# Optimization experiments

Measured on AMD Instinct MI355X. Metric: run time of the kernel, lower is better.

Reference implementation:

```python
import jax, jax.numpy as jnp
import numpy as np

H = 4096      # hidden_size
NH = 32       # num query heads
NKV = 2       # multi_query_group_num (kv heads)
HD = 128      # head_dim
ROT = 64      # rotary_dim = head_dim // 2
B, S = 2, 2048
QKV = (NH + 2 * NKV) * HD  # 4608
BASE = 10000.0


def apply_rope(x, pos):
    """GPT-J style (non-neox, interleaved) rope on first ROT dims of head_dim.
    x: [B,S,n,HD], pos: [B,S] int."""
    half = ROT // 2  # 32 frequency pairs
    inv_freq = 1.0 / (BASE ** (jnp.arange(0, ROT, 2, dtype=jnp.float32) / ROT))  # [half]
    freqs = pos.astype(jnp.float32)[..., None] * inv_freq        # [B,S,half]
    cos = jnp.cos(freqs)[:, :, None, :]                          # [B,S,1,half]
    sin = jnp.sin(freqs)[:, :, None, :]
    xr, xp = x[..., :ROT], x[..., ROT:]
    x1 = xr[..., 0::2]   # [B,S,n,half]
    x2 = xr[..., 1::2]
    o1 = x1 * cos - x2 * sin
    o2 = x2 * cos + x1 * sin
    rot = jnp.stack([o1, o2], axis=-1).reshape(x.shape[:-1] + (ROT,))
    return jnp.concatenate([rot, xp], axis=-1)


def setup_inputs() -> dict:
    key = jax.random.key(0)
    k1, k2, k3, k4 = jax.random.split(key, 4)
    hidden_states = jax.random.normal(k1, (B, S, H), dtype=jnp.float32)
    position_ids = jnp.broadcast_to(jnp.arange(S, dtype=jnp.int64), (B, S))
    Wqkv = jax.random.normal(k2, (H, QKV), dtype=jnp.float32) * 0.02
    bqkv = jax.random.normal(k3, (QKV,), dtype=jnp.float32) * 0.02
    Wo = jax.random.normal(k4, (NH * HD, H), dtype=jnp.float32) * 0.02
    return {"hidden_states": hidden_states, "position_ids": position_ids,
            "Wqkv": Wqkv, "bqkv": bqkv, "Wo": Wo}


def reference(hidden_states, position_ids, Wqkv, bqkv, Wo):
    qkv = hidden_states @ Wqkv + bqkv                      # [B,S,QKV]
    q = qkv[..., : NH * HD].reshape(B, S, NH, HD)
    k = qkv[..., NH * HD : (NH + NKV) * HD].reshape(B, S, NKV, HD)
    v = qkv[..., (NH + NKV) * HD :].reshape(B, S, NKV, HD)

    q = apply_rope(q, position_ids)
    k = apply_rope(k, position_ids)

    # GQA: expand kv heads to match query heads
    rep = NH // NKV
    k = jnp.repeat(k, rep, axis=2)   # [B,S,NH,HD]
    v = jnp.repeat(v, rep, axis=2)

    scale = HD ** -0.5
    scores = jnp.einsum("bqhd,bkhd->bhqk", q, k) * scale   # [B,NH,S,S]
    causal = jnp.tril(jnp.ones((S, S), dtype=bool))
    scores = jnp.where(causal, scores, jnp.finfo(scores.dtype).min)
    probs = jax.nn.softmax(scores, axis=-1)
    ctx = jnp.einsum("bhqk,bkhd->bqhd", probs, v).reshape(B, S, NH * HD)
    return ctx @ Wo                                        # [B,S,H]
```

## Files before the change

### kernel.cpp

```cpp
#include <hip/hip_runtime.h>
#include <stdint.h>

#define B_    2
#define S_    2048
#define H_    4096
#define NH_   32
#define NKV_  2
#define HD_   128
#define ROT_  64
#define QKVD  4608
#define MROWS 4096

typedef __attribute__((ext_vector_type(8))) __bf16 bf16x8;
typedef __attribute__((ext_vector_type(4))) float f32x4;

__device__ __forceinline__ unsigned short f2bf(float f) {
    union { float f; unsigned u; } c; c.f = f;
    unsigned u = c.u;
    u += 0x7fffu + ((u >> 16) & 1u);
    return (unsigned short)(u >> 16);
}

__device__ __forceinline__ void gload_lds16(const void* g, void* l) {
    __builtin_amdgcn_global_load_lds(
        (__attribute__((address_space(1))) void*)g,
        (__attribute__((address_space(3))) void*)l, 16, 0, 0);
}

__global__ __launch_bounds__(256) void convert_bf16(const float* __restrict__ src,
                                                    unsigned short* __restrict__ dst,
                                                    int n4) {
    int i = blockIdx.x * 256 + threadIdx.x;
    if (i < n4) {
        f32x4 v = ((const f32x4*)src)[i];
        ushort4 o;
        o.x = f2bf(v[0]); o.y = f2bf(v[1]); o.z = f2bf(v[2]); o.w = f2bf(v[3]);
        ((ushort4*)dst)[i] = o;
    }
}

__global__ __launch_bounds__(256) void transpose_bf16(const float* __restrict__ src,
                                                      unsigned short* __restrict__ dst,
                                                      int K, int N) {
    __shared__ float tile[32][33];
    int n0 = blockIdx.x * 32, k0 = blockIdx.y * 32;
    int tx = threadIdx.x & 31, ty = threadIdx.x >> 5;
#pragma unroll
    for (int i = 0; i < 4; i++)
        tile[ty + i * 8][tx] = src[(size_t)(k0 + ty + i * 8) * N + n0 + tx];
    __syncthreads();
#pragma unroll
    for (int i = 0; i < 4; i++)
        dst[(size_t)(n0 + ty + i * 8) * K + k0 + tx] = f2bf(tile[tx][ty + i * 8]);
}

template <int HAS_BIAS>
__global__ __launch_bounds__(256) void gemm_bt(const unsigned short* __restrict__ A,
                                               const unsigned short* __restrict__ BT,
                                               const float* __restrict__ bias,
                                               float* __restrict__ C,
                                               int M, int N, int K) {
    __shared__ __align__(16) unsigned short As[128 * 32];
    __shared__ __align__(16) unsigned short Bs[128 * 32];
    int tid = threadIdx.x;
    int lane = tid & 63, wave = tid >> 6;
    int quad = lane >> 4, lrow = lane & 15;
    int m0 = blockIdx.y * 128, n0 = blockIdx.x * 128;
    int wm = (wave >> 1) * 64, wn = (wave & 1) * 64;

    f32x4 acc[4][4];
#pragma unroll
    for (int mt = 0; mt < 4; mt++)
#pragma unroll
        for (int nt = 0; nt < 4; nt++) acc[mt][nt] = (f32x4){0.f, 0.f, 0.f, 0.f};

    int li0 = tid, li1 = 256 + tid;
    const unsigned short* ga0 = A + (size_t)(m0 + (li0 >> 2)) * K + (li0 & 3) * 8;
    const unsigned short* ga1 = A + (size_t)(m0 + (li1 >> 2)) * K + (li1 & 3) * 8;
    const unsigned short* gb0 = BT + (size_t)(n0 + (li0 >> 2)) * K + (li0 & 3) * 8;
    const unsigned short* gb1 = BT + (size_t)(n0 + (li1 >> 2)) * K + (li1 & 3) * 8;
    unsigned short* la0 = &As[(li0 & ~63) * 8];
    unsigned short* la1 = &As[(li1 & ~63) * 8];
    unsigned short* lb0 = &Bs[(li0 & ~63) * 8];
    unsigned short* lb1 = &Bs[(li1 & ~63) * 8];

    for (int k0 = 0; k0 < K; k0 += 32) {
        gload_lds16(ga0 + k0, la0);
        gload_lds16(ga1 + k0, la1);
        gload_lds16(gb0 + k0, lb0);
        gload_lds16(gb1 + k0, lb1);
        __syncthreads();
        bf16x8 af[4], bfr[4];
#pragma unroll
        for (int mt = 0; mt < 4; mt++)
            af[mt] = *(const bf16x8*)&As[(wm + mt * 16 + lrow) * 32 + quad * 8];
#pragma unroll
        for (int nt = 0; nt < 4; nt++)
            bfr[nt] = *(const bf16x8*)&Bs[(wn + nt * 16 + lrow) * 32 + quad * 8];
#pragma unroll
        for (int mt = 0; mt < 4; mt++)
#pragma unroll
            for (int nt = 0; nt < 4; nt++)
                acc[mt][nt] = __builtin_amdgcn_mfma_f32_16x16x32_bf16(af[mt], bfr[nt],
                                                                      acc[mt][nt], 0, 0, 0);
        __syncthreads();
    }
#pragma unroll
    for (int mt = 0; mt < 4; mt++) {
        int gm = m0 + wm + mt * 16 + quad * 4;
#pragma unroll
        for (int nt = 0; nt < 4; nt++) {
            int gn = n0 + wn + nt * 16 + lrow;
            float bv = HAS_BIAS ? bias[gn] : 0.f;
#pragma unroll
            for (int r = 0; r < 4; r++)
                C[(size_t)(gm + r) * N + gn] = acc[mt][nt][r] + bv;
        }
    }
}

__global__ __launch_bounds__(256) void gemm_qkv(const unsigned short* __restrict__ A,
                                                const unsigned short* __restrict__ BT,
                                                const float* __restrict__ bias,
                                                unsigned short* __restrict__ Qb,
                                                unsigned short* __restrict__ Kb,
                                                unsigned short* __restrict__ Vb) {
    const int K = H_;
    __shared__ __align__(16) unsigned short As[128 * 32];
    __shared__ __align__(16) unsigned short Bs[128 * 32];
    int tid = threadIdx.x;
    int lane = tid & 63, wave = tid >> 6;
    int quad = lane >> 4, lrow = lane & 15;
    int m0 = blockIdx.y * 128, n0 = blockIdx.x * 128;
    int head = blockIdx.x;
    int wm = (wave >> 1) * 64, wn = (wave & 1) * 64;

    f32x4 acc[4][4];
#pragma unroll
    for (int mt = 0; mt < 4; mt++)
#pragma unroll
        for (int nt = 0; nt < 4; nt++) acc[mt][nt] = (f32x4){0.f, 0.f, 0.f, 0.f};

    int li0 = tid, li1 = 256 + tid;
    const unsigned short* ga0 = A + (size_t)(m0 + (li0 >> 2)) * K + (li0 & 3) * 8;
    const unsigned short* ga1 = A + (size_t)(m0 + (li1 >> 2)) * K + (li1 & 3) * 8;
    const unsigned short* gb0 = BT + (size_t)(n0 + (li0 >> 2)) * K + (li0 & 3) * 8;
    const unsigned short* gb1 = BT + (size_t)(n0 + (li1 >> 2)) * K + (li1 & 3) * 8;
    unsigned short* la0 = &As[(li0 & ~63) * 8];
    unsigned short* la1 = &As[(li1 & ~63) * 8];
    unsigned short* lb0 = &Bs[(li0 & ~63) * 8];
    unsigned short* lb1 = &Bs[(li1 & ~63) * 8];

    for (int k0 = 0; k0 < K; k0 += 32) {
        gload_lds16(ga0 + k0, la0);
        gload_lds16(ga1 + k0, la1);
        gload_lds16(gb0 + k0, lb0);
        gload_lds16(gb1 + k0, lb1);
        __syncthreads();
        bf16x8 af[4], bfr[4];
#pragma unroll
        for (int mt = 0; mt < 4; mt++)
            af[mt] = *(const bf16x8*)&As[(wm + mt * 16 + lrow) * 32 + quad * 8];
#pragma unroll
        for (int nt = 0; nt < 4; nt++)
            bfr[nt] = *(const bf16x8*)&Bs[(wn + nt * 16 + lrow) * 32 + quad * 8];
#pragma unroll
        for (int mt = 0; mt < 4; mt++)
#pragma unroll
            for (int nt = 0; nt < 4; nt++)
                acc[mt][nt] = __builtin_amdgcn_mfma_f32_16x16x32_bf16(af[mt], bfr[nt],
                                                                      acc[mt][nt], 0, 0, 0);
        __syncthreads();
    }

    const float QSCALE = 0.08838834764831843f * 1.4426950408889634f;
#pragma unroll
    for (int mt = 0; mt < 4; mt++) {
        int gm = m0 + wm + mt * 16 + quad * 4;
        int bb = gm >> 11;
        int srow = gm & (S_ - 1);
#pragma unroll
        for (int nt = 0; nt < 4; nt++) {
            int dcol = wn + nt * 16 + lrow;
            float bv = bias[n0 + dcol];
            float vals[4];
#pragma unroll
            for (int r = 0; r < 4; r++) vals[r] = acc[mt][nt][r] + bv;
            if (head < 34 && dcol < ROT_) {
                int p = dcol >> 1;
                float inv = exp2f(-(float)p * 0.41524101186092035f);
                int odd = dcol & 1;
#pragma unroll
                for (int r = 0; r < 4; r++) {
                    float partner = __shfl_xor(vals[r], 1);
                    float sn, cs;
                    __sincosf((float)(srow + r) * inv, &sn, &cs);
                    vals[r] = odd ? (vals[r] * cs + partner * sn)
                                  : (vals[r] * cs - partner * sn);
                }
            }
            if (head < 32) {
                unsigned short* dst =
                    Qb + ((size_t)(bb * NH_ + head) * S_ + srow) * HD_ + dcol;
#pragma unroll
                for (int r = 0; r < 4; r++) dst[r * HD_] = f2bf(vals[r] * QSCALE);
            } else if (head < 34) {
                size_t base = ((size_t)(bb * NKV_ + head - 32) * S_ + srow) * HD_;
#pragma unroll
                for (int r = 0; r < 4; r++)
                    Kb[base + r * HD_ + (((dcol >> 3) ^ ((srow + r) & 7)) << 3) +
                       (dcol & 7)] = f2bf(vals[r]);
            } else {
                size_t base = ((size_t)(bb * NKV_ + head - 34) * HD_ + dcol) * S_;
#pragma unroll
                for (int r = 0; r < 4; r++) {
                    int s = srow + r;
                    Vb[base + ((s >> 6) << 6) + ((((s >> 3) & 7) ^ (dcol & 7)) << 3) +
                       (s & 7)] = f2bf(vals[r]);
                }
            }
        }
    }
}

__global__ __launch_bounds__(256, 4) void flash4(const unsigned short* __restrict__ Qb,
                                                 const unsigned short* __restrict__ Kb,
                                                 const unsigned short* __restrict__ Vb,
                                                 unsigned short* __restrict__ ctxb) {
    int pair = blockIdx.x;
    int h = blockIdx.y, b = blockIdx.z;
    int tid = threadIdx.x, lane = tid & 63, wave = tid >> 6;
    int quad = lane >> 4, lrow = lane & 15;
    int bkvh = b * NKV_ + (h >> 4);
    int lw3 = lrow & 7;

    __shared__ __align__(16) unsigned short Ks[64 * 128];
    __shared__ __align__(16) unsigned short Vt[128 * 64];
    __shared__ __align__(16) unsigned short Ps[4][16 * 64];

    const unsigned short* Kg = Kb + (size_t)bkvh * S_ * HD_;
    const unsigned short* Vg = Vb + (size_t)bkvh * HD_ * S_;

#pragma unroll 1
    for (int u = 0; u < 2; u++) {
        int qblk = u ? ((int)(S_ / 64) - 1 - pair) : pair;
        int q0 = qblk * 64 + wave * 16;

        bf16x8 qf[4];
        {
            const unsigned short* qr =
                Qb + ((size_t)(b * NH_ + h) * S_ + q0 + lrow) * HD_ + quad * 8;
#pragma unroll
            for (int c = 0; c < 4; c++) qf[c] = *(const bf16x8*)(qr + c * 32);
        }

        float m_i[4], l_i[4];
        f32x4 oacc[8];
#pragma unroll
        for (int r = 0; r < 4; r++) { m_i[r] = -1e30f; l_i[r] = 0.f; }
#pragma unroll
        for (int t = 0; t < 8; t++) oacc[t] = (f32x4){0.f, 0.f, 0.f, 0.f};

        int nkt = qblk + 1;
#pragma unroll 1
        for (int kt = 0; kt < nkt; kt++) {
            int ks0 = kt * 64;
            {
                const unsigned short* g =
                    Kg + (size_t)(ks0 + wave * 16 + (lane >> 4)) * HD_ + (lane & 15) * 8;
                unsigned short* l = &Ks[wave * 16 * 128];
#pragma unroll
                for (int i = 0; i < 4; i++)
                    gload_lds16(g + i * 4 * 128, l + i * 4 * 128);
            }
            {
                const unsigned short* g =
                    Vg + (size_t)(wave * 32 + (lane >> 3)) * S_ + ks0 + (lane & 7) * 8;
                unsigned short* l = &Vt[wave * 32 * 64];
#pragma unroll
                for (int i = 0; i < 4; i++)
                    gload_lds16(g + (size_t)i * 8 * S_, l + i * 8 * 64);
            }
            __syncthreads();

            if (ks0 <= q0 + 15) {
                f32x4 s[4];
#pragma unroll
                for (int n = 0; n < 4; n++) s[n] = (f32x4){0.f, 0.f, 0.f, 0.f};
#pragma unroll
                for (int kc = 0; kc < 4; kc++)
#pragma unroll
                    for (int n = 0; n < 4; n++) {
                        bf16x8 kf = *(const bf16x8*)
                            &Ks[(n * 16 + lrow) * 128 + (((kc * 4 + quad) ^ lw3) << 3)];
                        s[n] = __builtin_amdgcn_mfma_f32_16x16x32_bf16(qf[kc], kf, s[n],
                                                                       0, 0, 0);
                    }
                if (kt == nkt - 1) {
#pragma unroll
                    for (int n = 0; n < 4; n++)
#pragma unroll
                        for (int r = 0; r < 4; r++)
                            if (ks0 + n * 16 + lrow > q0 + quad * 4 + r)
                                s[n][r] = -1e30f;
                }
                float alpha[4];
#pragma unroll
                for (int r = 0; r < 4; r++) {
                    float mx = fmaxf(fmaxf(s[0][r], s[1][r]), fmaxf(s[2][r], s[3][r]));
                    mx = fmaxf(mx, __shfl_xor(mx, 1));
                    mx = fmaxf(mx, __shfl_xor(mx, 2));
                    mx = fmaxf(mx, __shfl_xor(mx, 4));
                    mx = fmaxf(mx, __shfl_xor(mx, 8));
                    float mn = fmaxf(m_i[r], mx);
                    alpha[r] = exp2f(m_i[r] - mn);
                    m_i[r] = mn;
                    float rs = 0.f;
#pragma unroll
                    for (int n = 0; n < 4; n++) {
                        s[n][r] = exp2f(s[n][r] - mn);
                        rs += s[n][r];
                    }
                    rs += __shfl_xor(rs, 1);
                    rs += __shfl_xor(rs, 2);
                    rs += __shfl_xor(rs, 4);
                    rs += __shfl_xor(rs, 8);
                    l_i[r] = l_i[r] * alpha[r] + rs;
                }
#pragma unroll
                for (int n = 0; n < 4; n++)
#pragma unroll
                    for (int r = 0; r < 4; r++) {
                        int rw = quad * 4 + r, col = n * 16 + lrow;
                        Ps[wave][rw * 64 + (((col >> 3) ^ (rw & 7)) << 3) + (col & 7)] =
                            f2bf(s[n][r]);
                    }
#pragma unroll
                for (int t = 0; t < 8; t++)
#pragma unroll
                    for (int r = 0; r < 4; r++) oacc[t][r] *= alpha[r];
                bf16x8 pf0 = *(const bf16x8*)&Ps[wave][lrow * 64 + ((quad ^ lw3) << 3)];
                bf16x8 pf1 = *(const bf16x8*)&Ps[wave][lrow * 64 + (((4 + quad) ^ lw3) << 3)];
#pragma unroll
                for (int t = 0; t < 8; t++) {
                    int dim = t * 16 + lrow;
                    bf16x8 v0 = *(const bf16x8*)&Vt[dim * 64 + ((quad ^ lw3) << 3)];
                    bf16x8 v1 = *(const bf16x8*)&Vt[dim * 64 + (((4 + quad) ^ lw3) << 3)];
                    oacc[t] = __builtin_amdgcn_mfma_f32_16x16x32_bf16(pf0, v0, oacc[t], 0, 0, 0);
                    oacc[t] = __builtin_amdgcn_mfma_f32_16x16x32_bf16(pf1, v1, oacc[t], 0, 0, 0);
                }
            }
            __syncthreads();
        }
        float inv[4];
#pragma unroll
        for (int r = 0; r < 4; r++) inv[r] = 1.f / l_i[r];
#pragma unroll
        for (int t = 0; t < 8; t++)
#pragma unroll
            for (int r = 0; r < 4; r++) {
                int q = q0 + quad * 4 + r;
                ctxb[(size_t)(b * S_ + q) * (NH_ * HD_) + h * HD_ + t * 16 + lrow] =
                    f2bf(oacc[t][r] * inv[r]);
            }
    }
}

extern "C" void kernel_launch(void* const* d_in, const int* in_sizes, int n_in,
                              void* d_out, int out_size, void* d_ws, size_t ws_size,
                              hipStream_t stream) {
    const float* hidden = (const float*)d_in[0];
    const float* Wqkv = (const float*)d_in[2];
    const float* bqkv = (const float*)d_in[3];
    const float* Wo   = (const float*)d_in[4];
    float* out = (float*)d_out;

    char* ws = (char*)d_ws;
    unsigned short* Xb    = (unsigned short*)ws;
    unsigned short* WqkvT = (unsigned short*)(ws + 33554432);
    unsigned short* Qb    = (unsigned short*)(ws + 71303168);
    unsigned short* Kb    = (unsigned short*)(ws + 104857600);
    unsigned short* Vb    = (unsigned short*)(ws + 106954752);
    unsigned short* ctxb  = (unsigned short*)(ws + 109051904);
    unsigned short* WoT   = Xb;

    convert_bf16<<<16384, 256, 0, stream>>>(hidden, Xb, (MROWS * H_) / 4);
    transpose_bf16<<<dim3(QKVD / 32, H_ / 32), 256, 0, stream>>>(Wqkv, WqkvT, H_, QKVD);
    gemm_qkv<<<dim3(QKVD / 128, MROWS / 128), 256, 0, stream>>>(Xb, WqkvT, bqkv,
                                                                Qb, Kb, Vb);
    transpose_bf16<<<dim3(H_ / 32, H_ / 32), 256, 0, stream>>>(Wo, WoT, NH_ * HD_, H_);
    flash4<<<dim3(S_ / 128, NH_, B_), 256, 0, stream>>>(Qb, Kb, Vb, ctxb);
    gemm_bt<0><<<dim3(H_ / 128, MROWS / 128), 256, 0, stream>>>(ctxb, WoT, nullptr, out,
                                                                MROWS, H_, NH_ * HD_);
}
```

Measured before the change: 837.7 us.

## Replace both GEMMs with 256x256 tiled, multi-buffered pipelined MFMA kernel

Both projection GEMMs are replaced by one templated kernel that uses 256x256 block tiles, 512 threads and 128KB of dynamic LDS. The K tile grows to 64 with an XOR-swizzled layout to avoid bank conflicts. Global-to-LDS loads for later K steps are issued while MFMAs run on the current buffers, with explicit vmcnt waits, barriers and setprio around the MFMA phases. The goal is to hide memory latency and raise data reuse per tile compared with the old single-buffered 128x128 loop. The cost is more LDS per block, lower occupancy and hardcoded K=4096 strides.

```diff
diff --git a/kernel.cpp b/kernel.cpp
--- a/kernel.cpp
+++ b/kernel.cpp
@@ -54,174 +54,212 @@
         dst[(size_t)(n0 + ty + i * 8) * K + k0 + tx] = f2bf(tile[tx][ty + i * 8]);
 }
 
-template <int HAS_BIAS>
-__global__ __launch_bounds__(256) void gemm_bt(const unsigned short* __restrict__ A,
-                                               const unsigned short* __restrict__ BT,
-                                               const float* __restrict__ bias,
-                                               float* __restrict__ C,
-                                               int M, int N, int K) {
-    __shared__ __align__(16) unsigned short As[128 * 32];
-    __shared__ __align__(16) unsigned short Bs[128 * 32];
-    int tid = threadIdx.x;
-    int lane = tid & 63, wave = tid >> 6;
-    int quad = lane >> 4, lrow = lane & 15;
-    int m0 = blockIdx.y * 128, n0 = blockIdx.x * 128;
-    int wm = (wave >> 1) * 64, wn = (wave & 1) * 64;
-
-    f32x4 acc[4][4];
-#pragma unroll
-    for (int mt = 0; mt < 4; mt++)
-#pragma unroll
-        for (int nt = 0; nt < 4; nt++) acc[mt][nt] = (f32x4){0.f, 0.f, 0.f, 0.f};
-
-    int li0 = tid, li1 = 256 + tid;
-    const unsigned short* ga0 = A + (size_t)(m0 + (li0 >> 2)) * K + (li0 & 3) * 8;
-    const unsigned short* ga1 = A + (size_t)(m0 + (li1 >> 2)) * K + (li1 & 3) * 8;
-    const unsigned short* gb0 = BT + (size_t)(n0 + (li0 >> 2)) * K + (li0 & 3) * 8;
-    const unsigned short* gb1 = BT + (size_t)(n0 + (li1 >> 2)) * K + (li1 & 3) * 8;
-    unsigned short* la0 = &As[(li0 & ~63) * 8];
-    unsigned short* la1 = &As[(li1 & ~63) * 8];
-    unsigned short* lb0 = &Bs[(li0 & ~63) * 8];
-    unsigned short* lb1 = &Bs[(li1 & ~63) * 8];
-
-    for (int k0 = 0; k0 < K; k0 += 32) {
-        gload_lds16(ga0 + k0, la0);
-        gload_lds16(ga1 + k0, la1);
-        gload_lds16(gb0 + k0, lb0);
-        gload_lds16(gb1 + k0, lb1);
-        __syncthreads();
-        bf16x8 af[4], bfr[4];
-#pragma unroll
-        for (int mt = 0; mt < 4; mt++)
-            af[mt] = *(const bf16x8*)&As[(wm + mt * 16 + lrow) * 32 + quad * 8];
-#pragma unroll
-        for (int nt = 0; nt < 4; nt++)
-            bfr[nt] = *(const bf16x8*)&Bs[(wn + nt * 16 + lrow) * 32 + quad * 8];
-#pragma unroll
-        for (int mt = 0; mt < 4; mt++)
-#pragma unroll
-            for (int nt = 0; nt < 4; nt++)
-                acc[mt][nt] = __builtin_amdgcn_mfma_f32_16x16x32_bf16(af[mt], bfr[nt],
-                                                                      acc[mt][nt], 0, 0, 0);
-        __syncthreads();
+
+__device__ __forceinline__ void stage_half(const unsigned short* g,
+                                           unsigned short* slot,
+                                           int kt, int tid, int wave) {
+    int ko = (kt < 64 ? kt : 63) << 6;
+#pragma unroll
+    for (int j = 0; j < 2; j++) {
+        int li = j * 512 + tid;
+        int r = li >> 3, s = li & 7;
+        gload_lds16(g + ((size_t)r << 12) + ko + ((s ^ (r & 7)) << 3),
+                    slot + (size_t)(j * 512 + wave * 64) * 8);
     }
-#pragma unroll
-    for (int mt = 0; mt < 4; mt++) {
-        int gm = m0 + wm + mt * 16 + quad * 4;
-#pragma unroll
-        for (int nt = 0; nt < 4; nt++) {
-            int gn = n0 + wn + nt * 16 + lrow;
-            float bv = HAS_BIAS ? bias[gn] : 0.f;
-#pragma unroll
-            for (int r = 0; r < 4; r++)
-                C[(size_t)(gm + r) * N + gn] = acc[mt][nt][r] + bv;
-        }
+}
+
+template <int PAR, int MH>
+__device__ __forceinline__ void lda_frags(const unsigned short* lds, bf16x8 (&af)[4][2],
+                                          int wm, int lrow, int quad, int lw) {
+    const unsigned short* p = lds + (PAR * 2 + MH) * 8192 + (wm * 64 + lrow) * 64;
+#pragma unroll
+    for (int mf = 0; mf < 4; mf++)
+#pragma unroll
+        for (int ks = 0; ks < 2; ks++)
+            af[mf][ks] = *(const bf16x8*)(p + mf * 1024 + (((ks * 4 + quad) ^ lw) << 3));
+}
+
+template <int PAR, int NH>
+__device__ __forceinline__ void ldb_frags(const unsigned short* lds, bf16x8 (&bf)[2][2],
+                                          int wn, int lrow, int quad, int lw) {
+    const unsigned short* p =
+        lds + 32768 + (PAR * 2 + NH) * 8192 + (wn * 32 + lrow) * 64;
+#pragma unroll
+    for (int nf = 0; nf < 2; nf++)
+#pragma unroll
+        for (int ks = 0; ks < 2; ks++)
+            bf[nf][ks] = *(const bf16x8*)(p + nf * 1024 + (((ks * 4 + quad) ^ lw) << 3));
+}
+
+template <int MH, int NH>
+__device__ __forceinline__ void mfma_quad(f32x4 (&acc)[8][4], const bf16x8 (&af)[4][2],
+                                          const bf16x8 (&bf)[2][2]) {
+#pragma unroll
+    for (int mf = 0; mf < 4; mf++)
+#pragma unroll
+        for (int nf = 0; nf < 2; nf++)
+#pragma unroll
+            for (int ks = 0; ks < 2; ks++)
+                acc[MH * 4 + mf][NH * 2 + nf] = __builtin_amdgcn_mfma_f32_16x16x32_bf16(
+                    af[mf][ks], bf[nf][ks], acc[MH * 4 + mf][NH * 2 + nf], 0, 0, 0);
+}
+
+#define MMPH(MH, NH, BF)                                   \
+    __builtin_amdgcn_s_barrier();                          \
+    asm volatile("s_waitcnt lgkmcnt(0)" ::: "memory");     \
+    __builtin_amdgcn_s_setprio(1);                         \
+    mfma_quad<MH, NH>(acc, af, BF);                        \
+    __builtin_amdgcn_s_setprio(0);
+
+template <int EPI, int N>
+__global__ __launch_bounds__(512, 2) void gemm256(const unsigned short* __restrict__ A,
+                                                  const unsigned short* __restrict__ BT,
+                                                  const float* __restrict__ bias,
+                                                  float* __restrict__ C,
+                                                  unsigned short* __restrict__ Qb,
+                                                  unsigned short* __restrict__ Kb,
+                                                  unsigned short* __restrict__ Vb) {
+    extern __shared__ unsigned short lds[];
+    const int tid = threadIdx.x;
+    const int lane = tid & 63, wave = tid >> 6;
+    const int wm = wave >> 2, wn = wave & 3;
+    const int quad = lane >> 4, lrow = lane & 15, lw = lrow & 7;
+    const int m0 = blockIdx.y * 256, n0 = blockIdx.x * 256;
+    const unsigned short* gA0 = A + ((size_t)m0 << 12);
+    const unsigned short* gA1 = gA0 + ((size_t)128 << 12);
+    const unsigned short* gB0 = BT + ((size_t)n0 << 12);
+    const unsigned short* gB1 = gB0 + ((size_t)128 << 12);
+
+    f32x4 acc[8][4];
+#pragma unroll
+    for (int i = 0; i < 8; i++)
+#pragma unroll
+        for (int j = 0; j < 4; j++) acc[i][j] = (f32x4){0.f, 0.f, 0.f, 0.f};
+    bf16x8 af[4][2], bf0[2][2], bf1[2][2];
+
+    stage_half(gA0, lds,                 0, tid, wave);
+    stage_half(gB0, lds + 32768,         0, tid, wave);
+    stage_half(gA1, lds + 8192,          0, tid, wave);
+    stage_half(gB1, lds + 32768 + 8192,  0, tid, wave);
+    stage_half(gA0, lds + 16384,         1, tid, wave);
+    stage_half(gB0, lds + 32768 + 16384, 1, tid, wave);
+    asm volatile("s_waitcnt vmcnt(4)" ::: "memory");
+    __builtin_amdgcn_s_barrier();
+
+#pragma unroll 1
+    for (int i = 0; i < 32; ++i) {
+        const int t0 = 2 * i;
+        lda_frags<0, 0>(lds, af, wm, lrow, quad, lw);
+        ldb_frags<0, 0>(lds, bf0, wn, lrow, quad, lw);
+        stage_half(gA1, lds + 24576, t0 + 1, tid, wave);
+        MMPH(0, 0, bf0);
+        __builtin_amdgcn_s_barrier();
+        ldb_frags<0, 1>(lds, bf1, wn, lrow, quad, lw);
+        stage_half(gB1, lds + 32768 + 24576, t0 + 1, tid, wave);
+        MMPH(0, 1, bf1);
+        __builtin_amdgcn_s_barrier();
+        lda_frags<0, 1>(lds, af, wm, lrow, quad, lw);
+        stage_half(gA0, lds, t0 + 2, tid, wave);
+        MMPH(1, 0, bf0);
+        __builtin_amdgcn_s_barrier();
+        stage_half(gB0, lds + 32768, t0 + 2, tid, wave);
+        MMPH(1, 1, bf1);
+        asm volatile("s_waitcnt vmcnt(4)" ::: "memory");
+        __builtin_amdgcn_s_barrier();
+        lda_frags<1, 0>(lds, af, wm, lrow, quad, lw);
+        ldb_frags<1, 0>(lds, bf0, wn, lrow, quad, lw);
+        stage_half(gA1, lds + 8192, t0 + 2, tid, wave);
+        MMPH(0, 0, bf0);
+        __builtin_amdgcn_s_barrier();
+        ldb_frags<1, 1>(lds, bf1, wn, lrow, quad, lw);
+        stage_half(gB1, lds + 32768 + 8192, t0 + 2, tid, wave);
+        MMPH(0, 1, bf1);
+        __builtin_amdgcn_s_barrier();
+        lda_frags<1, 1>(lds, af, wm, lrow, quad, lw);
+        stage_half(gA0, lds + 16384, t0 + 3, tid, wave);
+        MMPH(1, 0, bf0);
+        __builtin_amdgcn_s_barrier();
+        stage_half(gB0, lds + 32768 + 16384, t0 + 3, tid, wave);
+        MMPH(1, 1, bf1);
+        asm volatile("s_waitcnt vmcnt(4)" ::: "memory");
+        __builtin_amdgcn_s_barrier();
     }
-}
-
-__global__ __launch_bounds__(256) void gemm_qkv(const unsigned short* __restrict__ A,
-                                                const unsigned short* __restrict__ BT,
-                                                const float* __restrict__ bias,
-                                                unsigned short* __restrict__ Qb,
-                                                unsigned short* __restrict__ Kb,
-                                                unsigned short* __restrict__ Vb) {
-    const int K = H_;
-    __shared__ __align__(16) unsigned short As[128 * 32];
-    __shared__ __align__(16) unsigned short Bs[128 * 32];
-    int tid = threadIdx.x;
-    int lane = tid & 63, wave = tid >> 6;
-    int quad = lane >> 4, lrow = lane & 15;
-    int m0 = blockIdx.y * 128, n0 = blockIdx.x * 128;
-    int head = blockIdx.x;
-    int wm = (wave >> 1) * 64, wn = (wave & 1) * 64;
-
-    f32x4 acc[4][4];
-#pragma unroll
-    for (int mt = 0; mt < 4; mt++)
-#pragma unroll
-        for (int nt = 0; nt < 4; nt++) acc[mt][nt] = (f32x4){0.f, 0.f, 0.f, 0.f};
-
-    int li0 = tid, li1 = 256 + tid;
-    const unsigned short* ga0 = A + (size_t)(m0 + (li0 >> 2)) * K + (li0 & 3) * 8;
-    const unsigned short* ga1 = A + (size_t)(m0 + (li1 >> 2)) * K + (li1 & 3) * 8;
-    const unsigned short* gb0 = BT + (size_t)(n0 + (li0 >> 2)) * K + (li0 & 3) * 8;
-    const unsigned short* gb1 = BT + (size_t)(n0 + (li1 >> 2)) * K + (li1 & 3) * 8;
-    unsigned short* la0 = &As[(li0 & ~63) * 8];
-    unsigned short* la1 = &As[(li1 & ~63) * 8];
-    unsigned short* lb0 = &Bs[(li0 & ~63) * 8];
-    unsigned short* lb1 = &Bs[(li1 & ~63) * 8];
-
-    for (int k0 = 0; k0 < K; k0 += 32) {
-        gload_lds16(ga0 + k0, la0);
-        gload_lds16(ga1 + k0, la1);
-        gload_lds16(gb0 + k0, lb0);
-        gload_lds16(gb1 + k0, lb1);
-        __syncthreads();
-        bf16x8 af[4], bfr[4];
-#pragma unroll
-        for (int mt = 0; mt < 4; mt++)
-            af[mt] = *(const bf16x8*)&As[(wm + mt * 16 + lrow) * 32 + quad * 8];
-#pragma unroll
-        for (int nt = 0; nt < 4; nt++)
-            bfr[nt] = *(const bf16x8*)&Bs[(wn + nt * 16 + lrow) * 32 + quad * 8];
-#pragma unroll
-        for (int mt = 0; mt < 4; mt++)
-#pragma unroll
-            for (int nt = 0; nt < 4; nt++)
-                acc[mt][nt] = __builtin_amdgcn_mfma_f32_16x16x32_bf16(af[mt], bfr[nt],
-                                                                      acc[mt][nt], 0, 0, 0);
-        __syncthreads();
+
+    if constexpr (EPI == 0) {
+#pragma unroll
+        for (int mh = 0; mh < 2; mh++)
+#pragma unroll
+            for (int mf = 0; mf < 4; mf++) {
+                int gm = m0 + mh * 128 + wm * 64 + mf * 16 + quad * 4;
+#pragma unroll
+                for (int nh = 0; nh < 2; nh++)
+#pragma unroll
+                    for (int nf = 0; nf < 2; nf++) {
+                        int gn = n0 + nh * 128 + wn * 32 + nf * 16 + lrow;
+#pragma unroll
+                        for (int r = 0; r < 4; r++)
+                            C[(size_t)(gm + r) * N + gn] = acc[mh * 4 + mf][nh * 2 + nf][r];
+                    }
+            }
+    } else {
+        const float QSCALE = 0.08838834764831843f * 1.4426950408889634f;
+#pragma unroll
+        for (int mh = 0; mh < 2; mh++)
+#pragma unroll
+            for (int mf = 0; mf < 4; mf++) {
+                int gm = m0 + mh * 128 + wm * 64 + mf * 16 + quad * 4;
+                int bb = gm >> 11;
+                int srow = gm & (S_ - 1);
+#pragma unroll
+                for (int nh = 0; nh < 2; nh++)
+#pragma unroll
+                    for (int nf = 0; nf < 2; nf++) {
+                        int colF = n0 + nh * 128 + wn * 32 + nf * 16 + lrow;
+                        int head = colF >> 7, dcol = colF & 127;
+                        float bv = bias[colF];
+                        float vals[4];
+#pragma unroll
+                        for (int r = 0; r < 4; r++)
+                            vals[r] = acc[mh * 4 + mf][nh * 2 + nf][r] + bv;
+                        if (head < 34 && dcol < ROT_) {
+                            int p = dcol >> 1;
+                            float inv = exp2f(-(float)p * 0.41524101186092035f);
+                            int odd = dcol & 1;
+#pragma unroll
+                            for (int r = 0; r < 4; r++) {
+                                float partner = __shfl_xor(vals[r], 1);
+                                float sn, cs;
+                                __sincosf((float)(srow + r) * inv, &sn, &cs);
+                                vals[r] = odd ? (vals[r] * cs + partner * sn)
+                                              : (vals[r] * cs - partner * sn);
+                            }
+                        }
+                        if (head < 32) {
+                            unsigned short* dst =
+                                Qb + ((size_t)(bb * NH_ + head) * S_ + srow) * HD_ + dcol;
+#pragma unroll
+                            for (int r = 0; r < 4; r++) dst[r * HD_] = f2bf(vals[r] * QSCALE);
+                        } else if (head < 34) {
+                            size_t base = ((size_t)(bb * NKV_ + head - 32) * S_ + srow) * HD_;
+#pragma unroll
+                            for (int r = 0; r < 4; r++)
+                                Kb[base + r * HD_ + (((dcol >> 3) ^ ((srow + r) & 7)) << 3) +
+                                   (dcol & 7)] = f2bf(vals[r]);
+                        } else {
+                            size_t base = ((size_t)(bb * NKV_ + head - 34) * HD_ + dcol) * S_;
+#pragma unroll
+                            for (int r = 0; r < 4; r++) {
+                                int s = srow + r;
+                                Vb[base + ((s >> 6) << 6) +
+                                   ((((s >> 3) & 7) ^ (dcol & 7)) << 3) + (s & 7)] =
+                                    f2bf(vals[r]);
+                            }
+                        }
+                    }
+            }
     }
-
-    const float QSCALE = 0.08838834764831843f * 1.4426950408889634f;
-#pragma unroll
-    for (int mt = 0; mt < 4; mt++) {
-        int gm = m0 + wm + mt * 16 + quad * 4;
-        int bb = gm >> 11;
-        int srow = gm & (S_ - 1);
-#pragma unroll
-        for (int nt = 0; nt < 4; nt++) {
-            int dcol = wn + nt * 16 + lrow;
-            float bv = bias[n0 + dcol];
-            float vals[4];
-#pragma unroll
-            for (int r = 0; r < 4; r++) vals[r] = acc[mt][nt][r] + bv;
-            if (head < 34 && dcol < ROT_) {
-                int p = dcol >> 1;
-                float inv = exp2f(-(float)p * 0.41524101186092035f);
-                int odd = dcol & 1;
-#pragma unroll
-                for (int r = 0; r < 4; r++) {
-                    float partner = __shfl_xor(vals[r], 1);
-                    float sn, cs;
-                    __sincosf((float)(srow + r) * inv, &sn, &cs);
-                    vals[r] = odd ? (vals[r] * cs + partner * sn)
-                                  : (vals[r] * cs - partner * sn);
-                }
-            }
-            if (head < 32) {
-                unsigned short* dst =
-                    Qb + ((size_t)(bb * NH_ + head) * S_ + srow) * HD_ + dcol;
-#pragma unroll
-                for (int r = 0; r < 4; r++) dst[r * HD_] = f2bf(vals[r] * QSCALE);
-            } else if (head < 34) {
-                size_t base = ((size_t)(bb * NKV_ + head - 32) * S_ + srow) * HD_;
-#pragma unroll
-                for (int r = 0; r < 4; r++)
-                    Kb[base + r * HD_ + (((dcol >> 3) ^ ((srow + r) & 7)) << 3) +
-                       (dcol & 7)] = f2bf(vals[r]);
-            } else {
-                size_t base = ((size_t)(bb * NKV_ + head - 34) * HD_ + dcol) * S_;
-#pragma unroll
-                for (int r = 0; r < 4; r++) {
-                    int s = srow + r;
-                    Vb[base + ((s >> 6) << 6) + ((((s >> 3) & 7) ^ (dcol & 7)) << 3) +
-                       (s & 7)] = f2bf(vals[r]);
-                }
-            }
-        }
-    }
-}
+}
+#undef MMPH
 
 __global__ __launch_bounds__(256, 4) void flash4(const unsigned short* __restrict__ Qb,
                                                  const unsigned short* __restrict__ Kb,
@@ -386,10 +424,10 @@
 
     convert_bf16<<<16384, 256, 0, stream>>>(hidden, Xb, (MROWS * H_) / 4);
     transpose_bf16<<<dim3(QKVD / 32, H_ / 32), 256, 0, stream>>>(Wqkv, WqkvT, H_, QKVD);
-    gemm_qkv<<<dim3(QKVD / 128, MROWS / 128), 256, 0, stream>>>(Xb, WqkvT, bqkv,
-                                                                Qb, Kb, Vb);
+    gemm256<1, QKVD><<<dim3(QKVD / 256, MROWS / 256), 512, 131072, stream>>>(
+        Xb, WqkvT, bqkv, nullptr, Qb, Kb, Vb);
     transpose_bf16<<<dim3(H_ / 32, H_ / 32), 256, 0, stream>>>(Wo, WoT, NH_ * HD_, H_);
     flash4<<<dim3(S_ / 128, NH_, B_), 256, 0, stream>>>(Qb, Kb, Vb, ctxb);
-    gemm_bt<0><<<dim3(H_ / 128, MROWS / 128), 256, 0, stream>>>(ctxb, WoT, nullptr, out,
-                                                                MROWS, H_, NH_ * HD_);
-}
+    gemm256<0, H_><<<dim3(H_ / 256, MROWS / 256), 512, 131072, stream>>>(
+        ctxb, WoT, nullptr, out, nullptr, nullptr, nullptr);
+}
```

Result: faster. 711.2 us (-15.1%).
